# Kernel tuning notes

Hardware: AMD Instinct MI355X
Metric: run time of the kernel (lower is better)

The kernel has to match this reference:

```python
import jax, jax.numpy as jnp
import numpy as np
from jax import lax

# Per-tensor power-of-two scales (ScalingImplType.CONST / POWER_OF_TWO in Brevitas)
S_ACT8 = 2.0 ** -4   # 8-bit signed input quant scale
S_ACT4 = 2.0 ** -1   # 4-bit signed input quant scale
S_W = 2.0 ** -2      # per-tensor weight quant scale
S_RELU = 2.0 ** -2   # 4-bit unsigned QuantReLU scale


def fq(x, scale, qmin, qmax):
    # fake-quant with straight-through estimator (STE)
    q = jnp.clip(jnp.round(x / scale), qmin, qmax) * scale
    return x + lax.stop_gradient(q - x)


def fq_signed(x, scale, bits):
    return fq(x, scale, -(2 ** (bits - 1)), 2 ** (bits - 1) - 1)


def fq_uint(x, scale, bits):
    return fq(x, scale, 0, 2 ** bits - 1)


def qconv(x, w, in_bits, w_bits, s_in, stride=1, padding=0, groups=1):
    xq = fq_signed(x, s_in, in_bits)
    wq = fq_signed(w, S_W, w_bits)
    return lax.conv_general_dilated(
        xq, wq, (stride, stride), [(padding, padding)] * 2,
        feature_group_count=groups,
        dimension_numbers=('NCHW', 'OIHW', 'NCHW'))


def maxpool(x, k, s):
    return lax.reduce_window(x, -jnp.inf, lax.max,
                             (1, 1, k, k), (1, 1, s, s), 'VALID')


def dwsep(x, dw, pw):
    c = x.shape[1]
    x = qconv(x, dw, 4, 4, S_ACT4, padding=1, groups=c)  # depthwise 3x3
    x = qconv(x, pw, 4, 4, S_ACT4)                       # pointwise 1x1
    return x


def qrelu4(x):
    return fq_uint(jax.nn.relu(x), S_RELU, 4)


def setup_inputs() -> dict:
    key = jax.random.key(0)
    ks = jax.random.split(key, 10)
    B = 1024
    mk = lambda k, shp, sc=0.5: jax.random.normal(k, shp, jnp.float32) * sc
    return {
        'x': jax.random.normal(ks[0], (B, 3, 32, 32), jnp.float32),
        'w0': mk(ks[1], (3, 3, 1, 1)),
        'dw1': mk(ks[2], (3, 1, 3, 3)),
        'pw1': mk(ks[3], (32, 3, 1, 1)),
        'dw2': mk(ks[4], (32, 1, 3, 3)),
        'pw2': mk(ks[5], (64, 32, 1, 1)),
        'dw3': mk(ks[6], (64, 1, 3, 3)),
        'pw3': mk(ks[7], (128, 64, 1, 1)),
        'wc1': mk(ks[8], (256, 128, 1, 1)),
        'wc2': mk(ks[9], (10, 256, 1, 1)),
    }


def reference(x, w0, dw1, pw1, dw2, pw2, dw3, pw3, wc1, wc2):
    # features
    h = qconv(x, w0, 8, 8, S_ACT8)            # 1x1, 3->3, 8-bit
    h = dwsep(h, dw1, pw1)                    # 3->32, 32x32
    h = qrelu4(h)
    h = maxpool(h, 2, 2)                      # 16x16
    h = dwsep(h, dw2, pw2)                    # 32->64
    h = qrelu4(h)
    h = maxpool(h, 2, 2)                      # 8x8
    h = dwsep(h, dw3, pw3)                    # 64->128
    h = qrelu4(h)
    h = maxpool(h, 8, 1)                      # 1x1
    # classifier
    h = qconv(h, wc1, 4, 4, S_ACT4)           # 128->256
    h = qrelu4(h)
    h = qconv(h, wc2, 4, 4, S_ACT4)           # 256->10
    h = fq_signed(h, S_ACT8, 8)               # output quant int8
    return h
```

## Files before the change

kernel.cpp:

```cpp
#include <hip/hip_runtime.h>

typedef int v4i __attribute__((ext_vector_type(4)));

#define W0i   0
#define DW1i  9
#define PW1i  36
#define DW2i  132
#define PW1pk 132
#define DW1pk 164
#define WC1p  3556
#define WC2p  11748
#define PW2Fb 12388
#define PW3Fb 12900
#define DW2pk 14948
#define DW3pk 15092
#define WTOT  15380

__device__ __attribute__((aligned(16))) int g_wsq[WTOT];

__device__ __forceinline__ int iclamp(int v, int lo, int hi) {
  return v < lo ? lo : (v > hi ? hi : v);
}
__device__ __forceinline__ int rne4(int a) {
  return (a + 1 + ((a >> 2) & 1)) >> 2;
}
__device__ __forceinline__ int rne32(int a) {
  return (a + 15 + ((a >> 5) & 1)) >> 5;
}

__device__ __forceinline__ void bar_lds() {
  asm volatile("s_waitcnt lgkmcnt(0)\n\ts_barrier" ::: "memory");
}

__device__ __forceinline__ int dot4(int a, int b, int c) {
#if defined(__has_builtin) && __has_builtin(__builtin_amdgcn_sdot4)
  return __builtin_amdgcn_sdot4(a, b, c, false);
#else
  c += ((a << 24) >> 24) * ((b << 24) >> 24);
  c += ((a << 16) >> 24) * ((b << 16) >> 24);
  c += ((a <<  8) >> 24) * ((b <<  8) >> 24);
  c += (a >> 24) * (b >> 24);
  return c;
#endif
}

__device__ __forceinline__ int alignb(int hi, int lo, int sh) {
#if defined(__has_builtin) && __has_builtin(__builtin_amdgcn_alignbyte)
  return __builtin_amdgcn_alignbyte(hi, lo, sh);
#else
  return (int)(((((unsigned long long)(unsigned)hi) << 32) |
                (unsigned)lo) >> (8 * sh));
#endif
}

__device__ __forceinline__ int pack3(int a, int b, int c) {
  return (a & 0xff) | ((b & 0xff) << 8) | ((c & 0xff) << 16);
}
__device__ __forceinline__ int q4w(float w) {
  return iclamp((int)rintf(w * 4.f), -8, 7);
}

__device__ __forceinline__ int pk_mad16(int a, int b, int c) {
  int d;
  asm("v_pk_mad_i16 %0, %1, %2, %3" : "=v"(d) : "v"(a), "v"(b), "v"(c));
  return d;
}
__device__ __forceinline__ int pk_add16(int a, int b) {
  int d;
  asm("v_pk_add_i16 %0, %1, %2" : "=v"(d) : "v"(a), "v"(b));
  return d;
}
__device__ __forceinline__ int pk_ashr16(int sh, int a) {
  int d;
  asm("v_pk_ashrrev_i16 %0, %1, %2" : "=v"(d) : "v"(sh), "v"(a));
  return d;
}
__device__ __forceinline__ int pk_max16(int a, int b) {
  int d;
  asm("v_pk_max_i16 %0, %1, %2" : "=v"(d) : "v"(a), "v"(b));
  return d;
}
__device__ __forceinline__ int pk_min16(int a, int b) {
  int d;
  asm("v_pk_min_i16 %0, %1, %2" : "=v"(d) : "v"(a), "v"(b));
  return d;
}
__device__ __forceinline__ int rne4s_pk(int a) {
  const int sh = 0x00020002, one = 0x00010001;
  int t = pk_ashr16(sh, a);
  t &= one;
  t += one;
  int s4 = pk_add16(a, t);
  int r = pk_ashr16(sh, s4);
  r = pk_max16(r, (int)0xFFF8FFF8);
  r = pk_min16(r, 0x00070007);
  return r;
}

__device__ __forceinline__ int max4(v4i d) {
  int a = d[0] > d[1] ? d[0] : d[1];
  int b = d[2] > d[3] ? d[2] : d[3];
  return a > b ? a : b;
}

__global__ __launch_bounds__(256) void prep_weights(
    const float* __restrict__ w0,  const float* __restrict__ dw1,
    const float* __restrict__ pw1, const float* __restrict__ dw2,
    const float* __restrict__ pw2, const float* __restrict__ dw3,
    const float* __restrict__ pw3, const float* __restrict__ wc1,
    const float* __restrict__ wc2) {
  int t = blockIdx.x * blockDim.x + threadIdx.x;
  if (t >= WTOT) return;
  if (t < DW2i) {
    float w; int lo = -8, hi = 7;
    if (t < DW1i)      { w = w0[t];        lo = -128; hi = 127; }
    else if (t < PW1i)   w = dw1[t - DW1i];
    else                 w = pw1[t - PW1i];
    g_wsq[t] = iclamp((int)rintf(w * 4.f), lo, hi);
  } else if (t < PW1pk + 32) {
    int o = t - PW1pk;
    g_wsq[t] = pack3(q4w(pw1[3 * o]), q4w(pw1[3 * o + 1]), q4w(pw1[3 * o + 2]));
  } else if (t < DW1pk + 9) {
    int i = t - DW1pk;
    g_wsq[t] = pack3(q4w(dw1[3 * i]), q4w(dw1[3 * i + 1]), q4w(dw1[3 * i + 2]));
  } else if (t < WC1p) {
    return;
  } else if (t < PW2Fb) {
    const float* src = (t < WC2p) ? wc1 + (t - WC1p) * 4
                                  : wc2 + (t - WC2p) * 4;
    int p = 0;
#pragma unroll
    for (int b = 0; b < 4; b++) {
      int c = iclamp((int)rintf(src[b] * 4.f), -8, 7);
      p |= (c & 0xff) << (8 * b);
    }
    g_wsq[t] = p;
  } else if (t < PW3Fb) {
    int i = t - PW2Fb;
    int nt = i >> 7, r = i & 127, lane = r >> 1, dw = r & 1;
    int n = nt * 16 + (lane & 15);
    int kb = (lane >> 4) * 8 + dw * 4;
    int p = 0;
#pragma unroll
    for (int b = 0; b < 4; b++) {
      int c = iclamp((int)rintf(pw2[n * 32 + kb + b] * 4.f), -8, 7);
      p |= (c & 0xff) << (8 * b);
    }
    g_wsq[t] = p;
  } else if (t < DW2pk) {
    int i = t - PW3Fb;
    int g = i >> 7, r = i & 127, lane = r >> 1, dw = r & 1;
    int nt = g >> 1, kh = g & 1;
    int n = nt * 16 + (lane & 15);
    int kb = kh * 32 + (lane >> 4) * 8 + dw * 4;
    int p = 0;
#pragma unroll
    for (int b = 0; b < 4; b++) {
      int c = iclamp((int)rintf(pw3[n * 64 + kb + b] * 4.f), -8, 7);
      p |= (c & 0xff) << (8 * b);
    }
    g_wsq[t] = p;
  } else if (t < DW3pk) {
    int i = t - DW2pk;
    int cq = i / 18, r = i - cq * 18, t9 = r >> 1, par = r & 1;
    int wl = q4w(dw2[(cq * 4 + par) * 9 + t9]);
    int wh = q4w(dw2[(cq * 4 + 2 + par) * 9 + t9]);
    g_wsq[t] = (wl & 0xFFFF) | (wh << 16);
  } else {
    int i = t - DW3pk;
    int cq = i / 18, r = i - cq * 18, t9 = r >> 1, par = r & 1;
    int wl = q4w(dw3[(cq * 4 + par) * 9 + t9]);
    int wh = q4w(dw3[(cq * 4 + 2 + par) * 9 + t9]);
    g_wsq[t] = (wl & 0xFFFF) | (wh << 16);
  }
}

__global__ __launch_bounds__(512, 8) void fused_net(
    const float* __restrict__ x,
    float* __restrict__ out)
{
  const int img = blockIdx.x;
  const int tid = threadIdx.x;
  const int wv = tid >> 6, lane = tid & 63;
  const int lm = lane & 15, kg = lane >> 4;
  const int* __restrict__ wq = g_wsq;

  __shared__ __align__(16) int bufAi[2560];
  __shared__ __align__(16) int bufBi[2592];

  const int ntp = (wv & 1) * 2;
  const long bw0 = *(const long*)(wq + PW2Fb + (ntp * 64 + lane) * 2);
  const long bw1 = *(const long*)(wq + PW2Fb + ((ntp + 1) * 64 + lane) * 2);
  const long b0v = *(const long*)(wq + PW3Fb + (wv * 2 + 0) * 128 + lane * 2);
  const long b1v = *(const long*)(wq + PW3Fb + (wv * 2 + 1) * 128 + lane * 2);

  if (tid < 256) {
    const float* xim = x + (size_t)img * 3072;
    const int p4 = tid * 4;
    float4 v0 = *(const float4*)(xim + p4);
    float4 v1 = *(const float4*)(xim + 1024 + p4);
    float4 v2 = *(const float4*)(xim + 2048 + p4);
    int w[9];
#pragma unroll
    for (int i = 0; i < 9; i++) w[i] = wq[W0i + i];
#define Q8(v) iclamp((int)rintf((v) * 16.f), -128, 127)
    int a0[4] = {Q8(v0.x), Q8(v0.y), Q8(v0.z), Q8(v0.w)};
    int a1[4] = {Q8(v1.x), Q8(v1.y), Q8(v1.z), Q8(v1.w)};
    int a2[4] = {Q8(v2.x), Q8(v2.y), Q8(v2.z), Q8(v2.w)};
#undef Q8
#pragma unroll
    for (int o = 0; o < 3; o++) {
      int pk = 0;
#pragma unroll
      for (int j = 0; j < 4; j++) {
        int s = a0[j] * w[o * 3] + a1[j] * w[o * 3 + 1] + a2[j] * w[o * 3 + 2];
        pk |= (iclamp(rne32(s), -8, 7) & 0xff) << (8 * j);
      }
      bufAi[o * 256 + tid] = pk;
    }
  }
  bar_lds();

  {
    const int pos = tid & 255, half = tid >> 8;
    const int py = pos >> 4, px = pos & 15;
    int wr[3][3], wrh[3][3];
#pragma unroll
    for (int c = 0; c < 3; c++)
#pragma unroll
      for (int ky = 0; ky < 3; ky++) {
        int w = wq[DW1pk + c * 3 + ky];
        wr[c][ky] = w;
        wrh[c][ky] = w << 8;
      }
    const int s = (px & 1) ? 1 : 3;
    const int D0 = (2 * px - 1) >> 2;
    int V[3][4];
#pragma unroll
    for (int r = 0; r < 4; r++) {
      int rr = 2 * py - 1 + r;
      bool ok = (unsigned)rr < 32u;
#pragma unroll
      for (int c = 0; c < 3; c++) {
        int lo = 0, hi = 0;
        if (ok) {
          const int* ap = bufAi + c * 256 + rr * 8;
          if (px > 0)  lo = ap[D0];
          if (px < 15) hi = ap[D0 + 1];
        }
        V[c][r] = alignb(hi, lo, s);
      }
    }
    int a[4];
#pragma unroll
    for (int dy = 0; dy < 2; dy++) {
      int r01[3];
#pragma unroll
      for (int c = 0; c < 3; c++) {
        int acc0 = 0, acc1 = 0;
#pragma unroll
        for (int ky = 0; ky < 3; ky++) {
          acc0 = dot4(V[c][dy + ky], wr[c][ky], acc0);
          acc1 = dot4(V[c][dy + ky], wrh[c][ky], acc1);
        }
        int p = (int)__builtin_amdgcn_perm((unsigned)acc1, (unsigned)acc0,
                                           0x05040100u);
        r01[c] = rne4s_pk(p);
      }
      unsigned t0 = __builtin_amdgcn_perm((unsigned)r01[1], (unsigned)r01[0],
                                          0x0C0C0400u);
      a[2 * dy] = (int)__builtin_amdgcn_perm((unsigned)r01[2], t0, 0x0C040100u);
      unsigned t1 = __builtin_amdgcn_perm((unsigned)r01[1], (unsigned)r01[0],
                                          0x0C0C0602u);
      a[2 * dy + 1] =
          (int)__builtin_amdgcn_perm((unsigned)r01[2], t1, 0x0C060100u);
    }
#pragma unroll
    for (int it2 = 0; it2 < 4; it2++) {
      int it = half * 4 + it2;
      int pk = 0;
#pragma unroll
      for (int j = 0; j < 4; j++) {
        int wpk = wq[PW1pk + it * 4 + j];
        int m0 = dot4(a[0], wpk, 0), m1 = dot4(a[1], wpk, 0);
        int m2 = dot4(a[2], wpk, 0), m3 = dot4(a[3], wpk, 0);
        int mx = max(max(m0, m1), max(m2, m3));
        pk |= iclamp(rne4(mx), 0, 7) << (8 * j);
      }
      bufBi[py * 149 + px * 9 + it] = pk;
    }
  }
  bar_lds();

  {
    const int cq = tid >> 6;
    const int rem = tid & 63;
    const int y = rem >> 2, xq = rem & 3, x0 = xq * 4;
    int we[9], wo[9];
    {
      const int2* wp = (const int2*)(wq + DW2pk + cq * 18);
#pragma unroll
      for (int t9 = 0; t9 < 9; t9++) { int2 v = wp[t9]; we[t9] = v.x; wo[t9] = v.y; }
    }
    int acce[4] = {}, acco[4] = {};
#pragma unroll
    for (int ky = 0; ky < 3; ky++) {
      int yy = y + ky - 1;
      if (yy < 0 || yy > 15) continue;
      int rb = yy * 149 + cq;
      int rd[6];
      rd[0] = (x0 > 0) ? bufBi[rb + (x0 - 1) * 9] : 0;
#pragma unroll
      for (int k = 1; k < 5; k++) rd[k] = bufBi[rb + (x0 - 1 + k) * 9];
      rd[5] = (x0 < 12) ? bufBi[rb + (x0 + 4) * 9] : 0;
      int ee[6], eo[6];
#pragma unroll
      for (int k = 0; k < 6; k++) {
        ee[k] = rd[k] & 0x000F000F;
        eo[k] = (rd[k] >> 8) & 0x000F000F;
      }
#pragma unroll
      for (int j = 0; j < 4; j++)
#pragma unroll
        for (int kx = 0; kx < 3; kx++) {
          acce[j] = pk_mad16(ee[j + kx], we[ky * 3 + kx], acce[j]);
          acco[j] = pk_mad16(eo[j + kx], wo[ky * 3 + kx], acco[j]);
        }
    }
    const int py = y >> 1, dy = y & 1;
#pragma unroll
    for (int j = 0; j < 4; j++) {
      int xx = x0 + j;
      int qp = py * 8 + (xx >> 1);
      int q = qp ^ (py & 3);
      int m = q * 4 + dy * 2 + (xx & 1);
      int re = rne4s_pk(acce[j]);
      int ro = rne4s_pk(acco[j]);
      bufAi[m * 10 + cq] = (re & 0x00FF00FF) | ((ro & 0x00FF00FF) << 8);
    }
  }
  bar_lds();

  {
    const int mtb = (wv >> 1) * 4;
    const signed char* Ab = (const signed char*)bufAi;
    signed char* A2c = (signed char*)bufBi;
    const int n0 = ntp * 16 + lm, n1 = (ntp + 1) * 16 + lm;
#pragma unroll
    for (int mt = mtb; mt < mtb + 4; mt++) {
      int m = mt * 16 + lm;
      long av = *(const long*)(Ab + m * 40 + kg * 8);
      v4i d0 = __builtin_amdgcn_mfma_i32_16x16x32_i8(av, bw0, (v4i){0, 0, 0, 0},
                                                     0, 0, 0);
      v4i d1 = __builtin_amdgcn_mfma_i32_16x16x32_i8(av, bw1, (v4i){0, 0, 0, 0},
                                                     0, 0, 0);
      int q = mt * 4 + kg;
      int qp = q ^ ((q >> 3) & 3);
      int py = qp >> 3, px = qp & 7;
      int bb = (py * 137 + px * 17) * 4;
      A2c[bb + n0] = (signed char)iclamp(rne4(max4(d0)), 0, 7);
      A2c[bb + n1] = (signed char)iclamp(rne4(max4(d1)), 0, 7);
    }
  }
  bar_lds();

  {
    int cq2 = tid >> 5;
    int s = tid & 31;
    int y = s >> 2, x0 = (s & 3) << 1;
    int we[9], wo[9];
    {
      const int2* wp = (const int2*)(wq + DW3pk + cq2 * 18);
#pragma unroll
      for (int t9 = 0; t9 < 9; t9++) { int2 v = wp[t9]; we[t9] = v.x; wo[t9] = v.y; }
    }
    int acce[2] = {}, acco[2] = {};
#pragma unroll
    for (int ky = 0; ky < 3; ky++) {
      int yy = y + ky - 1;
      if (yy < 0 || yy > 7) continue;
      int rb = yy * 137 + cq2;
      int rd[4];
      rd[0] = (x0 > 0) ? bufBi[rb + (x0 - 1) * 17] : 0;
      rd[1] = bufBi[rb + x0 * 17];
      rd[2] = bufBi[rb + (x0 + 1) * 17];
      rd[3] = (x0 < 6) ? bufBi[rb + (x0 + 2) * 17] : 0;
      int ee[4], eo[4];
#pragma unroll
      for (int k = 0; k < 4; k++) {
        ee[k] = rd[k] & 0x000F000F;
        eo[k] = (rd[k] >> 8) & 0x000F000F;
      }
#pragma unroll
      for (int j = 0; j < 2; j++)
#pragma unroll
        for (int kx = 0; kx < 3; kx++) {
          acce[j] = pk_mad16(ee[j + kx], we[ky * 3 + kx], acce[j]);
          acco[j] = pk_mad16(eo[j + kx], wo[ky * 3 + kx], acco[j]);
        }
    }
#pragma unroll
    for (int j = 0; j < 2; j++) {
      int re = rne4s_pk(acce[j]);
      int ro = rne4s_pk(acco[j]);
      bufAi[(y * 8 + x0 + j) * 18 + cq2] =
          (re & 0x00FF00FF) | ((ro & 0x00FF00FF) << 8);
    }
  }
  int4 wfc[4];
  {
    const int o = tid >> 1, sub = tid & 1;
    const int4* wp = (const int4*)(wq + WC1p + o * 32 + sub * 16);
#pragma unroll
    for (int rI = 0; rI < 4; rI++) wfc[rI] = wp[rI];
  }
  bar_lds();

  {
    const signed char* Ab = (const signed char*)bufAi;
    signed char* fcin = (signed char*)bufBi;
    int mx = -1000000;
#pragma unroll
    for (int mt = 0; mt < 4; mt++) {
      int m = mt * 16 + lm;
      long a0 = *(const long*)(Ab + m * 72 + kg * 8);
      long a1 = *(const long*)(Ab + m * 72 + 32 + kg * 8);
      v4i d = __builtin_amdgcn_mfma_i32_16x16x32_i8(a0, b0v,
                                                    (v4i){0, 0, 0, 0}, 0, 0, 0);
      d = __builtin_amdgcn_mfma_i32_16x16x32_i8(a1, b1v, d, 0, 0, 0);
      int t4 = max4(d);
      mx = mx > t4 ? mx : t4;
    }
    int red = max(mx, __shfl_xor(mx, 16));
    red = max(red, __shfl_xor(red, 32));
    if (lane < 16)
      fcin[wv * 16 + lm] = (signed char)iclamp(rne4(red), 0, 7);
  }
  bar_lds();

  {
    const int o = tid >> 1, sub = tid & 1;
    const int4* mp = (const int4*)bufBi + sub * 4;
    int acc = 0;
#pragma unroll
    for (int rI = 0; rI < 4; rI++) {
      int4 a = mp[rI]; int4 w = wfc[rI];
      acc = dot4(a.x, w.x, acc); acc = dot4(a.y, w.y, acc);
      acc = dot4(a.z, w.z, acc); acc = dot4(a.w, w.w, acc);
    }
    acc += __shfl_xor(acc, 1);
    if (sub == 0)
      ((signed char*)bufAi)[o] = (signed char)iclamp(rne4(acc), 0, 7);
  }
  bar_lds();

  if (tid < 40) {
    int k = tid >> 2, j = tid & 3;
    const int4* wp = (const int4*)(wq + WC2p + k * 64 + j * 16);
    const int4* ap = (const int4*)bufAi;
    int acc = 0;
#pragma unroll
    for (int r = 0; r < 4; r++) {
      int4 a = ap[j * 4 + r]; int4 w = wp[r];
      acc = dot4(a.x, w.x, acc); acc = dot4(a.y, w.y, acc);
      acc = dot4(a.z, w.z, acc); acc = dot4(a.w, w.w, acc);
    }
    acc += __shfl_xor(acc, 1);
    acc += __shfl_xor(acc, 2);
    if (j == 0) {
      int code = iclamp(2 * acc, -128, 127);
      out[(size_t)img * 10 + k] = (float)code * 0.0625f;
    }
  }
}

extern "C" void kernel_launch(void* const* d_in, const int* in_sizes, int n_in,
                              void* d_out, int out_size, void* d_ws, size_t ws_size,
                              hipStream_t stream) {
  (void)d_ws; (void)ws_size; (void)in_sizes; (void)n_in; (void)out_size;
  const float* x   = (const float*)d_in[0];
  const float* w0  = (const float*)d_in[1];
  const float* dw1 = (const float*)d_in[2];
  const float* pw1 = (const float*)d_in[3];
  const float* dw2 = (const float*)d_in[4];
  const float* pw2 = (const float*)d_in[5];
  const float* dw3 = (const float*)d_in[6];
  const float* pw3 = (const float*)d_in[7];
  const float* wc1 = (const float*)d_in[8];
  const float* wc2 = (const float*)d_in[9];
  float* out = (float*)d_out;

  prep_weights<<<(WTOT + 255) / 256, 256, 0, stream>>>(
      w0, dw1, pw1, dw2, pw2, dw3, pw3, wc1, wc2);
  fused_net<<<1024, 512, 0, stream>>>(x, out);
}
```

Before: 93.45 us.

## Process two images per block to amortize weight loads and barriers

Each 512-thread block now handles two images instead of one. Every stage loops over both images, sharing the register-held weights (including newly hoisted pw1 packed weights), and the number of blocks is halved. This spreads weight fetches and barrier overhead across twice the work and keeps all threads busy in the first stage. In exchange it doubles LDS per block and lowers the occupancy hint from 8 to 4 blocks, so fewer blocks run concurrently and latency hiding may suffer.

```diff
diff --git a/kernel.cpp b/kernel.cpp
--- a/kernel.cpp
+++ b/kernel.cpp
@@ -5,7 +5,6 @@
 #define W0i   0
 #define DW1i  9
 #define PW1i  36
-#define DW2i  132
 #define PW1pk 132
 #define DW1pk 164
 #define WC1p  3556
@@ -111,7 +110,7 @@
     const float* __restrict__ wc2) {
   int t = blockIdx.x * blockDim.x + threadIdx.x;
   if (t >= WTOT) return;
-  if (t < DW2i) {
+  if (t < 132) {
     float w; int lo = -8, hi = 7;
     if (t < DW1i)      { w = w0[t];        lo = -128; hi = 127; }
     else if (t < PW1i)   w = dw1[t - DW1i];
@@ -175,18 +174,18 @@
   }
 }
 
-__global__ __launch_bounds__(512, 8) void fused_net(
+__global__ __launch_bounds__(512, 4) void fused_net(
     const float* __restrict__ x,
     float* __restrict__ out)
 {
-  const int img = blockIdx.x;
+  const int img0 = blockIdx.x * 2;
   const int tid = threadIdx.x;
   const int wv = tid >> 6, lane = tid & 63;
   const int lm = lane & 15, kg = lane >> 4;
   const int* __restrict__ wq = g_wsq;
 
-  __shared__ __align__(16) int bufAi[2560];
-  __shared__ __align__(16) int bufBi[2592];
+  __shared__ __align__(16) int bufAi[2][2560];
+  __shared__ __align__(16) int bufBi[2][2384];
 
   const int ntp = (wv & 1) * 2;
   const long bw0 = *(const long*)(wq + PW2Fb + (ntp * 64 + lane) * 2);
@@ -194,9 +193,10 @@
   const long b0v = *(const long*)(wq + PW3Fb + (wv * 2 + 0) * 128 + lane * 2);
   const long b1v = *(const long*)(wq + PW3Fb + (wv * 2 + 1) * 128 + lane * 2);
 
-  if (tid < 256) {
-    const float* xim = x + (size_t)img * 3072;
-    const int p4 = tid * 4;
+  {
+    const int ii = tid >> 8, p = tid & 255;
+    const float* xim = x + (size_t)(img0 + ii) * 3072;
+    const int p4 = p * 4;
     float4 v0 = *(const float4*)(xim + p4);
     float4 v1 = *(const float4*)(xim + 1024 + p4);
     float4 v2 = *(const float4*)(xim + 2048 + p4);
@@ -216,13 +216,13 @@
         int s = a0[j] * w[o * 3] + a1[j] * w[o * 3 + 1] + a2[j] * w[o * 3 + 2];
         pk |= (iclamp(rne32(s), -8, 7) & 0xff) << (8 * j);
       }
-      bufAi[o * 256 + tid] = pk;
-    }
-  }
-  bar_lds();
-
-  {
-    const int pos = tid & 255, half = tid >> 8;
+      bufAi[ii][o * 256 + p] = pk;
+    }
+  }
+  bar_lds();
+
+  {
+    const int half = tid >> 8, pos = tid & 255;
     const int py = pos >> 4, px = pos & 15;
     int wr[3][3], wrh[3][3];
 #pragma unroll
@@ -233,61 +233,69 @@
         wr[c][ky] = w;
         wrh[c][ky] = w << 8;
       }
+    int wpk16[16];
+#pragma unroll
+    for (int i = 0; i < 16; i++)
+      wpk16[i] = wq[PW1pk + half * 16 + i];
     const int s = (px & 1) ? 1 : 3;
     const int D0 = (2 * px - 1) >> 2;
-    int V[3][4];
-#pragma unroll
-    for (int r = 0; r < 4; r++) {
-      int rr = 2 * py - 1 + r;
-      bool ok = (unsigned)rr < 32u;
-#pragma unroll
-      for (int c = 0; c < 3; c++) {
-        int lo = 0, hi = 0;
-        if (ok) {
-          const int* ap = bufAi + c * 256 + rr * 8;
-          if (px > 0)  lo = ap[D0];
-          if (px < 15) hi = ap[D0 + 1];
+#pragma unroll
+    for (int ii = 0; ii < 2; ii++) {
+      int V[3][4];
+#pragma unroll
+      for (int r = 0; r < 4; r++) {
+        int rr = 2 * py - 1 + r;
+        bool ok = (unsigned)rr < 32u;
+#pragma unroll
+        for (int c = 0; c < 3; c++) {
+          int lo = 0, hi = 0;
+          if (ok) {
+            const int* ap = &bufAi[ii][c * 256 + rr * 8];
+            if (px > 0)  lo = ap[D0];
+            if (px < 15) hi = ap[D0 + 1];
+          }
+          V[c][r] = alignb(hi, lo, s);
         }
-        V[c][r] = alignb(hi, lo, s);
-      }
-    }
-    int a[4];
-#pragma unroll
-    for (int dy = 0; dy < 2; dy++) {
-      int r01[3];
-#pragma unroll
-      for (int c = 0; c < 3; c++) {
-        int acc0 = 0, acc1 = 0;
-#pragma unroll
-        for (int ky = 0; ky < 3; ky++) {
-          acc0 = dot4(V[c][dy + ky], wr[c][ky], acc0);
-          acc1 = dot4(V[c][dy + ky], wrh[c][ky], acc1);
+      }
+      int a[4];
+#pragma unroll
+      for (int dy = 0; dy < 2; dy++) {
+        int r01[3];
+#pragma unroll
+        for (int c = 0; c < 3; c++) {
+          int acc0 = 0, acc1 = 0;
+#pragma unroll
+          for (int ky = 0; ky < 3; ky++) {
+            acc0 = dot4(V[c][dy + ky], wr[c][ky], acc0);
+            acc1 = dot4(V[c][dy + ky], wrh[c][ky], acc1);
+          }
+          int p = (int)__builtin_amdgcn_perm((unsigned)acc1, (unsigned)acc0,
+                                             0x05040100u);
+          r01[c] = rne4s_pk(p);
         }
-        int p = (int)__builtin_amdgcn_perm((unsigned)acc1, (unsigned)acc0,
-                                           0x05040100u);
-        r01[c] = rne4s_pk(p);
-      }
-      unsigned t0 = __builtin_amdgcn_perm((unsigned)r01[1], (unsigned)r01[0],
-                                          0x0C0C0400u);
-      a[2 * dy] = (int)__builtin_amdgcn_perm((unsigned)r01[2], t0, 0x0C040100u);
-      unsigned t1 = __builtin_amdgcn_perm((unsigned)r01[1], (unsigned)r01[0],
-                                          0x0C0C0602u);
-      a[2 * dy + 1] =
-          (int)__builtin_amdgcn_perm((unsigned)r01[2], t1, 0x0C060100u);
-    }
-#pragma unroll
-    for (int it2 = 0; it2 < 4; it2++) {
-      int it = half * 4 + it2;
-      int pk = 0;
-#pragma unroll
-      for (int j = 0; j < 4; j++) {
-        int wpk = wq[PW1pk + it * 4 + j];
-        int m0 = dot4(a[0], wpk, 0), m1 = dot4(a[1], wpk, 0);
-        int m2 = dot4(a[2], wpk, 0), m3 = dot4(a[3], wpk, 0);
-        int mx = max(max(m0, m1), max(m2, m3));
-        pk |= iclamp(rne4(mx), 0, 7) << (8 * j);
-      }
-      bufBi[py * 149 + px * 9 + it] = pk;
+        unsigned t0 = __builtin_amdgcn_perm((unsigned)r01[1], (unsigned)r01[0],
+                                            0x0C0C0400u);
+        a[2 * dy] =
+            (int)__builtin_amdgcn_perm((unsigned)r01[2], t0, 0x0C040100u);
+        unsigned t1 = __builtin_amdgcn_perm((unsigned)r01[1], (unsigned)r01[0],
+                                            0x0C0C0602u);
+        a[2 * dy + 1] =
+            (int)__builtin_amdgcn_perm((unsigned)r01[2], t1, 0x0C060100u);
+      }
+#pragma unroll
+      for (int it2 = 0; it2 < 4; it2++) {
+        int it = half * 4 + it2;
+        int pk = 0;
+#pragma unroll
+        for (int j = 0; j < 4; j++) {
+          int wpk = wpk16[it2 * 4 + j];
+          int m0 = dot4(a[0], wpk, 0), m1 = dot4(a[1], wpk, 0);
+          int m2 = dot4(a[2], wpk, 0), m3 = dot4(a[3], wpk, 0);
+          int mx = max(max(m0, m1), max(m2, m3));
+          pk |= iclamp(rne4(mx), 0, 7) << (8 * j);
+        }
+        bufBi[ii][py * 149 + px * 9 + it] = pk;
+      }
     }
   }
   bar_lds();
@@ -302,64 +310,70 @@
 #pragma unroll
       for (int t9 = 0; t9 < 9; t9++) { int2 v = wp[t9]; we[t9] = v.x; wo[t9] = v.y; }
     }
-    int acce[4] = {}, acco[4] = {};
-#pragma unroll
-    for (int ky = 0; ky < 3; ky++) {
-      int yy = y + ky - 1;
-      if (yy < 0 || yy > 15) continue;
-      int rb = yy * 149 + cq;
-      int rd[6];
-      rd[0] = (x0 > 0) ? bufBi[rb + (x0 - 1) * 9] : 0;
-#pragma unroll
-      for (int k = 1; k < 5; k++) rd[k] = bufBi[rb + (x0 - 1 + k) * 9];
-      rd[5] = (x0 < 12) ? bufBi[rb + (x0 + 4) * 9] : 0;
-      int ee[6], eo[6];
-#pragma unroll
-      for (int k = 0; k < 6; k++) {
-        ee[k] = rd[k] & 0x000F000F;
-        eo[k] = (rd[k] >> 8) & 0x000F000F;
-      }
-#pragma unroll
-      for (int j = 0; j < 4; j++)
-#pragma unroll
-        for (int kx = 0; kx < 3; kx++) {
-          acce[j] = pk_mad16(ee[j + kx], we[ky * 3 + kx], acce[j]);
-          acco[j] = pk_mad16(eo[j + kx], wo[ky * 3 + kx], acco[j]);
+    const int py = y >> 1, dy = y & 1;
+#pragma unroll
+    for (int ii = 0; ii < 2; ii++) {
+      int acce[4] = {}, acco[4] = {};
+#pragma unroll
+      for (int ky = 0; ky < 3; ky++) {
+        int yy = y + ky - 1;
+        if (yy < 0 || yy > 15) continue;
+        int rb = yy * 149 + cq;
+        int rd[6];
+        rd[0] = (x0 > 0) ? bufBi[ii][rb + (x0 - 1) * 9] : 0;
+#pragma unroll
+        for (int k = 1; k < 5; k++) rd[k] = bufBi[ii][rb + (x0 - 1 + k) * 9];
+        rd[5] = (x0 < 12) ? bufBi[ii][rb + (x0 + 4) * 9] : 0;
+        int ee[6], eo[6];
+#pragma unroll
+        for (int k = 0; k < 6; k++) {
+          ee[k] = rd[k] & 0x000F000F;
+          eo[k] = (rd[k] >> 8) & 0x000F000F;
         }
-    }
-    const int py = y >> 1, dy = y & 1;
-#pragma unroll
-    for (int j = 0; j < 4; j++) {
-      int xx = x0 + j;
-      int qp = py * 8 + (xx >> 1);
-      int q = qp ^ (py & 3);
-      int m = q * 4 + dy * 2 + (xx & 1);
-      int re = rne4s_pk(acce[j]);
-      int ro = rne4s_pk(acco[j]);
-      bufAi[m * 10 + cq] = (re & 0x00FF00FF) | ((ro & 0x00FF00FF) << 8);
+#pragma unroll
+        for (int j = 0; j < 4; j++)
+#pragma unroll
+          for (int kx = 0; kx < 3; kx++) {
+            acce[j] = pk_mad16(ee[j + kx], we[ky * 3 + kx], acce[j]);
+            acco[j] = pk_mad16(eo[j + kx], wo[ky * 3 + kx], acco[j]);
+          }
+      }
+#pragma unroll
+      for (int j = 0; j < 4; j++) {
+        int xx = x0 + j;
+        int qp = py * 8 + (xx >> 1);
+        int q = qp ^ (py & 3);
+        int m = q * 4 + dy * 2 + (xx & 1);
+        int re = rne4s_pk(acce[j]);
+        int ro = rne4s_pk(acco[j]);
+        bufAi[ii][m * 10 + cq] = (re & 0x00FF00FF) | ((ro & 0x00FF00FF) << 8);
+      }
     }
   }
   bar_lds();
 
   {
     const int mtb = (wv >> 1) * 4;
-    const signed char* Ab = (const signed char*)bufAi;
-    signed char* A2c = (signed char*)bufBi;
     const int n0 = ntp * 16 + lm, n1 = (ntp + 1) * 16 + lm;
 #pragma unroll
-    for (int mt = mtb; mt < mtb + 4; mt++) {
-      int m = mt * 16 + lm;
-      long av = *(const long*)(Ab + m * 40 + kg * 8);
-      v4i d0 = __builtin_amdgcn_mfma_i32_16x16x32_i8(av, bw0, (v4i){0, 0, 0, 0},
-                                                     0, 0, 0);
-      v4i d1 = __builtin_amdgcn_mfma_i32_16x16x32_i8(av, bw1, (v4i){0, 0, 0, 0},
-                                                     0, 0, 0);
-      int q = mt * 4 + kg;
-      int qp = q ^ ((q >> 3) & 3);
-      int py = qp >> 3, px = qp & 7;
-      int bb = (py * 137 + px * 17) * 4;
-      A2c[bb + n0] = (signed char)iclamp(rne4(max4(d0)), 0, 7);
-      A2c[bb + n1] = (signed char)iclamp(rne4(max4(d1)), 0, 7);
+    for (int ii = 0; ii < 2; ii++) {
+      const signed char* Ab = (const signed char*)bufAi[ii];
+      signed char* A2c = (signed char*)bufBi[ii];
+#pragma unroll
+      for (int mt = mtb; mt < mtb + 4; mt++) {
+        int m = mt * 16 + lm;
+        long av = *(const long*)(Ab + m * 40 + kg * 8);
+        v4i d0 = __builtin_amdgcn_mfma_i32_16x16x32_i8(av, bw0,
+                                                       (v4i){0, 0, 0, 0}, 0, 0, 0);
+        v4i d1 = __builtin_amdgcn_mfma_i32_16x16x32_i8(av, bw1,
+                                                       (v4i){0, 0, 0, 0}, 0, 0, 0);
+        int q = mt * 4 + kg;
+        int qp = q ^ ((q >> 3) & 3);
+        int py = qp >> 3, px = qp & 7;
+        int bb = (py * 137 + px * 17) * 4;
+        A2c[bb + n0] = (signed char)iclamp(rne4(max4(d0)), 0, 7);
+        A2c[bb + n1] = (signed char)iclamp(rne4(max4(d1)), 0, 7);
+      }
     }
   }
   bar_lds();
@@ -374,37 +388,40 @@
 #pragma unroll
       for (int t9 = 0; t9 < 9; t9++) { int2 v = wp[t9]; we[t9] = v.x; wo[t9] = v.y; }
     }
-    int acce[2] = {}, acco[2] = {};
-#pragma unroll
-    for (int ky = 0; ky < 3; ky++) {
-      int yy = y + ky - 1;
-      if (yy < 0 || yy > 7) continue;
-      int rb = yy * 137 + cq2;
-      int rd[4];
-      rd[0] = (x0 > 0) ? bufBi[rb + (x0 - 1) * 17] : 0;
-      rd[1] = bufBi[rb + x0 * 17];
-      rd[2] = bufBi[rb + (x0 + 1) * 17];
-      rd[3] = (x0 < 6) ? bufBi[rb + (x0 + 2) * 17] : 0;
-      int ee[4], eo[4];
-#pragma unroll
-      for (int k = 0; k < 4; k++) {
-        ee[k] = rd[k] & 0x000F000F;
-        eo[k] = (rd[k] >> 8) & 0x000F000F;
-      }
-#pragma unroll
-      for (int j = 0; j < 2; j++)
-#pragma unroll
-        for (int kx = 0; kx < 3; kx++) {
-          acce[j] = pk_mad16(ee[j + kx], we[ky * 3 + kx], acce[j]);
-          acco[j] = pk_mad16(eo[j + kx], wo[ky * 3 + kx], acco[j]);
+#pragma unroll
+    for (int ii = 0; ii < 2; ii++) {
+      int acce[2] = {}, acco[2] = {};
+#pragma unroll
+      for (int ky = 0; ky < 3; ky++) {
+        int yy = y + ky - 1;
+        if (yy < 0 || yy > 7) continue;
+        int rb = yy * 137 + cq2;
+        int rd[4];
+        rd[0] = (x0 > 0) ? bufBi[ii][rb + (x0 - 1) * 17] : 0;
+        rd[1] = bufBi[ii][rb + x0 * 17];
+        rd[2] = bufBi[ii][rb + (x0 + 1) * 17];
+        rd[3] = (x0 < 6) ? bufBi[ii][rb + (x0 + 2) * 17] : 0;
+        int ee[4], eo[4];
+#pragma unroll
+        for (int k = 0; k < 4; k++) {
+          ee[k] = rd[k] & 0x000F000F;
+          eo[k] = (rd[k] >> 8) & 0x000F000F;
         }
-    }
-#pragma unroll
-    for (int j = 0; j < 2; j++) {
-      int re = rne4s_pk(acce[j]);
-      int ro = rne4s_pk(acco[j]);
-      bufAi[(y * 8 + x0 + j) * 18 + cq2] =
-          (re & 0x00FF00FF) | ((ro & 0x00FF00FF) << 8);
+#pragma unroll
+        for (int j = 0; j < 2; j++)
+#pragma unroll
+          for (int kx = 0; kx < 3; kx++) {
+            acce[j] = pk_mad16(ee[j + kx], we[ky * 3 + kx], acce[j]);
+            acco[j] = pk_mad16(eo[j + kx], wo[ky * 3 + kx], acco[j]);
+          }
+      }
+#pragma unroll
+      for (int j = 0; j < 2; j++) {
+        int re = rne4s_pk(acce[j]);
+        int ro = rne4s_pk(acco[j]);
+        bufAi[ii][(y * 8 + x0 + j) * 18 + cq2] =
+            (re & 0x00FF00FF) | ((ro & 0x00FF00FF) << 8);
+      }
     }
   }
   int4 wfc[4];
@@ -417,59 +434,69 @@
   bar_lds();
 
   {
-    const signed char* Ab = (const signed char*)bufAi;
-    signed char* fcin = (signed char*)bufBi;
-    int mx = -1000000;
-#pragma unroll
-    for (int mt = 0; mt < 4; mt++) {
-      int m = mt * 16 + lm;
-      long a0 = *(const long*)(Ab + m * 72 + kg * 8);
-      long a1 = *(const long*)(Ab + m * 72 + 32 + kg * 8);
-      v4i d = __builtin_amdgcn_mfma_i32_16x16x32_i8(a0, b0v,
-                                                    (v4i){0, 0, 0, 0}, 0, 0, 0);
-      d = __builtin_amdgcn_mfma_i32_16x16x32_i8(a1, b1v, d, 0, 0, 0);
-      int t4 = max4(d);
-      mx = mx > t4 ? mx : t4;
-    }
-    int red = max(mx, __shfl_xor(mx, 16));
-    red = max(red, __shfl_xor(red, 32));
-    if (lane < 16)
-      fcin[wv * 16 + lm] = (signed char)iclamp(rne4(red), 0, 7);
+#pragma unroll
+    for (int ii = 0; ii < 2; ii++) {
+      const signed char* Ab = (const signed char*)bufAi[ii];
+      signed char* fcin = (signed char*)bufBi[ii];
+      int mx = -1000000;
+#pragma unroll
+      for (int mt = 0; mt < 4; mt++) {
+        int m = mt * 16 + lm;
+        long a0 = *(const long*)(Ab + m * 72 + kg * 8);
+        long a1 = *(const long*)(Ab + m * 72 + 32 + kg * 8);
+        v4i d = __builtin_amdgcn_mfma_i32_16x16x32_i8(a0, b0v,
+                                                      (v4i){0, 0, 0, 0}, 0, 0, 0);
+        d = __builtin_amdgcn_mfma_i32_16x16x32_i8(a1, b1v, d, 0, 0, 0);
+        int t4 = max4(d);
+        mx = mx > t4 ? mx : t4;
+      }
+      int red = max(mx, __shfl_xor(mx, 16));
+      red = max(red, __shfl_xor(red, 32));
+      if (lane < 16)
+        fcin[wv * 16 + lm] = (signed char)iclamp(rne4(red), 0, 7);
+    }
   }
   bar_lds();
 
   {
     const int o = tid >> 1, sub = tid & 1;
-    const int4* mp = (const int4*)bufBi + sub * 4;
-    int acc = 0;
-#pragma unroll
-    for (int rI = 0; rI < 4; rI++) {
-      int4 a = mp[rI]; int4 w = wfc[rI];
-      acc = dot4(a.x, w.x, acc); acc = dot4(a.y, w.y, acc);
-      acc = dot4(a.z, w.z, acc); acc = dot4(a.w, w.w, acc);
-    }
-    acc += __shfl_xor(acc, 1);
-    if (sub == 0)
-      ((signed char*)bufAi)[o] = (signed char)iclamp(rne4(acc), 0, 7);
-  }
-  bar_lds();
-
-  if (tid < 40) {
-    int k = tid >> 2, j = tid & 3;
-    const int4* wp = (const int4*)(wq + WC2p + k * 64 + j * 16);
-    const int4* ap = (const int4*)bufAi;
-    int acc = 0;
-#pragma unroll
-    for (int r = 0; r < 4; r++) {
-      int4 a = ap[j * 4 + r]; int4 w = wp[r];
-      acc = dot4(a.x, w.x, acc); acc = dot4(a.y, w.y, acc);
-      acc = dot4(a.z, w.z, acc); acc = dot4(a.w, w.w, acc);
-    }
-    acc += __shfl_xor(acc, 1);
-    acc += __shfl_xor(acc, 2);
-    if (j == 0) {
-      int code = iclamp(2 * acc, -128, 127);
-      out[(size_t)img * 10 + k] = (float)code * 0.0625f;
+#pragma unroll
+    for (int ii = 0; ii < 2; ii++) {
+      const int4* mp = (const int4*)bufBi[ii] + sub * 4;
+      int acc = 0;
+#pragma unroll
+      for (int rI = 0; rI < 4; rI++) {
+        int4 a = mp[rI]; int4 w = wfc[rI];
+        acc = dot4(a.x, w.x, acc); acc = dot4(a.y, w.y, acc);
+        acc = dot4(a.z, w.z, acc); acc = dot4(a.w, w.w, acc);
+      }
+      acc += __shfl_xor(acc, 1);
+      if (sub == 0)
+        ((signed char*)bufAi[ii])[o] = (signed char)iclamp(rne4(acc), 0, 7);
+    }
+  }
+  bar_lds();
+
+  {
+    const int half = tid >> 8;
+    const int t = tid & 255;
+    if (t < 40) {
+      int k = t >> 2, j = t & 3;
+      const int4* wp = (const int4*)(wq + WC2p + k * 64 + j * 16);
+      const int4* ap = (const int4*)bufAi[half];
+      int acc = 0;
+#pragma unroll
+      for (int r = 0; r < 4; r++) {
+        int4 a = ap[j * 4 + r]; int4 w = wp[r];
+        acc = dot4(a.x, w.x, acc); acc = dot4(a.y, w.y, acc);
+        acc = dot4(a.z, w.z, acc); acc = dot4(a.w, w.w, acc);
+      }
+      acc += __shfl_xor(acc, 1);
+      acc += __shfl_xor(acc, 2);
+      if (j == 0) {
+        int code = iclamp(2 * acc, -128, 127);
+        out[(size_t)(img0 + half) * 10 + k] = (float)code * 0.0625f;
+      }
     }
   }
 }
@@ -492,5 +519,5 @@
 
   prep_weights<<<(WTOT + 255) / 256, 256, 0, stream>>>(
       w0, dw1, pw1, dw2, pw2, dw3, pw3, wc1, wc2);
-  fused_net<<<1024, 512, 0, stream>>>(x, out);
-}
+  fused_net<<<512, 512, 0, stream>>>(x, out);
+}
```

Measured after the change: 96.19 us. +2.9%, slower.
